# Optimization experiments

Measured on AMD Instinct MI355X. Metric: run time of the kernel, lower is better.

The kernel has to match this reference:

```python
import jax, jax.numpy as jnp
import numpy as np

B, T, H, LD, FFN, TED = 4, 4096, 8, 128, 512, 2048
D = H * LD
LN_EPS = 1e-5


def setup_inputs() -> dict:
    key = jax.random.key(0)
    ks = jax.random.split(key, 8)
    s = lambda k, shape, sc=0.02: jax.random.normal(k, shape, jnp.float32) * sc
    return dict(
        x=s(ks[0], (B, T, D), 1.0),
        emb=s(ks[1], (B, TED), 1.0),
        W1=s(ks[2], (H, LD, FFN)),   # per-head linear1 weights
        b1=jnp.zeros((H, FFN), jnp.float32),
        W2=s(ks[3], (H, FFN, LD)),   # per-head linear2 weights
        b2=jnp.zeros((H, LD), jnp.float32),
        ln_w=jnp.ones((D,), jnp.float32),
        ln_b=jnp.zeros((D,), jnp.float32),
        emb_W=s(ks[4], (TED, 2 * D)),
        emb_b=jnp.zeros((2 * D,), jnp.float32),
        out_W=s(ks[5], (D, D)),
        out_b=jnp.zeros((D,), jnp.float32),
    )


def reference(x, emb, W1, b1, W2, b2, ln_w, ln_b, emb_W, emb_b, out_W, out_b):
    Bx, Tx, Dx = x.shape
    Hx = W1.shape[0]
    xh = x.reshape(Bx, Tx, Hx, -1)                      # (B,T,H,ld)
    # batched per-head 2-layer MLP (replaces the Python loop over heads)
    h1 = jax.nn.gelu(jnp.einsum('bthd,hdf->bthf', xh, W1) + b1, approximate=False)
    y = jnp.einsum('bthf,hfd->bthd', h1, W2) + b2       # (B,T,H,ld)
    y = y.reshape(Bx, Tx, Dx)                            # concat over heads
    # StylizationBlock: SiLU -> Linear -> scale/shift; LN modulate; SiLU -> Linear
    emb_out = jax.nn.silu(emb) @ emb_W + emb_b           # (B, 2D)
    scale, shift = jnp.split(emb_out[:, None, :], 2, axis=-1)
    mu = jnp.mean(y, axis=-1, keepdims=True)
    var = jnp.var(y, axis=-1, keepdims=True)
    yn = (y - mu) * jax.lax.rsqrt(var + LN_EPS) * ln_w + ln_b
    h = yn * (1.0 + scale) + shift
    out = jax.nn.silu(h) @ out_W + out_b
    return x + out
```

## Files before the change

### kernel.cpp

```cpp
#include <hip/hip_runtime.h>
#include <hip/hip_bf16.h>
#include <math.h>

#define B_     4
#define T_     4096
#define H_     8
#define LD_    128
#define FFN_   512
#define D_     1024
#define TED_   2048
#define TWO_D_ 2048
#define NTOK_  (B_ * T_)
#define LN_EPS_ 1e-5f

#define WS_EMB_OFF   0
#define WS_IMG1_OFF  (64 * 1024)
#define WS_IMG2_OFF  ((64 << 10) + (1 << 20))
#define WS_IMGO_OFF  ((64 << 10) + (2 << 20))
#define WS_Y_OFF     (8 << 20)

typedef short bf16x8 __attribute__((ext_vector_type(8)));
typedef float f32x4  __attribute__((ext_vector_type(4)));
typedef float f32x16 __attribute__((ext_vector_type(16)));
typedef unsigned int u32x4 __attribute__((ext_vector_type(4)));

__device__ __forceinline__ float siluf(float v) {
  return v * __builtin_amdgcn_rcpf(1.0f + __expf(-v));
}
__device__ __forceinline__ float geluf(float v) {
  const float s  = v * 0.70710678118654752440f;
  const float ax = fabsf(s);
  const float t  = __builtin_amdgcn_rcpf(fmaf(0.3275911f, ax, 1.0f));
  const float e  = __expf(-ax * ax);
  float p = fmaf(1.061405429f, t, -1.453152027f);
  p = fmaf(p, t, 1.421413741f);
  p = fmaf(p, t, -0.284496736f);
  p = fmaf(p, t, 0.254829592f);
  p = p * t;
  const float erf_ax = fmaf(-p, e, 1.0f);
  const float erf_s  = copysignf(erf_ax, s);
  return 0.5f * v * (1.0f + erf_s);
}
__device__ __forceinline__ unsigned short f2bf(float v) {
  unsigned int u = __float_as_uint(v);
  u += 0x7fffu + ((u >> 16) & 1u);
  return (unsigned short)(u >> 16);
}
__device__ __forceinline__ unsigned int pack2(float a, float b) {
  return (unsigned int)f2bf(a) | ((unsigned int)f2bf(b) << 16);
}
__device__ __forceinline__ void unpack8(uint4 u, float* v) {
  v[0] = __uint_as_float(u.x << 16); v[1] = __uint_as_float(u.x & 0xffff0000u);
  v[2] = __uint_as_float(u.y << 16); v[3] = __uint_as_float(u.y & 0xffff0000u);
  v[4] = __uint_as_float(u.z << 16); v[5] = __uint_as_float(u.z & 0xffff0000u);
  v[6] = __uint_as_float(u.w << 16); v[7] = __uint_as_float(u.w & 0xffff0000u);
}

__device__ __forceinline__ void gload_lds16(const void* g, void* l) {
#pragma clang diagnostic push
#pragma clang diagnostic ignored "-Waddress-space-conversion"
  __builtin_amdgcn_global_load_lds(
      (const __attribute__((address_space(1))) unsigned int*)g,
      (__attribute__((address_space(3))) unsigned int*)l, 16, 0, 0);
#pragma clang diagnostic pop
}

__global__ __launch_bounds__(256) void k0_emb(
    const float* __restrict__ emb, const float* __restrict__ emb_W,
    const float* __restrict__ emb_b, float* __restrict__ emb_out) {
  __shared__ float se[B_][128];
  const int tid = threadIdx.x;
  const int j   = blockIdx.x * 256 + tid;
  const int k0  = blockIdx.y * 128;
  for (int i = tid; i < B_ * 128; i += 256) {
    const int b = i >> 7, k = i & 127;
    se[b][k] = siluf(emb[b * TED_ + k0 + k]);
  }
  __syncthreads();
  float a0 = 0.f, a1 = 0.f, a2 = 0.f, a3 = 0.f;
  const float* Wp = emb_W + (size_t)k0 * TWO_D_ + j;
  for (int k = 0; k < 128; ++k) {
    const float w = Wp[(size_t)k * TWO_D_];
    a0 += se[0][k] * w; a1 += se[1][k] * w;
    a2 += se[2][k] * w; a3 += se[3][k] * w;
  }
  if (blockIdx.y == 0) {
    const float bb = emb_b[j];
    a0 += bb; a1 += bb; a2 += bb; a3 += bb;
  }
  atomicAdd(&emb_out[0 * TWO_D_ + j], a0);
  atomicAdd(&emb_out[1 * TWO_D_ + j], a1);
  atomicAdd(&emb_out[2 * TWO_D_ + j], a2);
  atomicAdd(&emb_out[3 * TWO_D_ + j], a3);
}

__global__ __launch_bounds__(256) void kprep(
    const float* __restrict__ W1, const float* __restrict__ W2,
    const float* __restrict__ out_W,
    unsigned short* __restrict__ img1, unsigned short* __restrict__ img2,
    unsigned short* __restrict__ imgO) {
  const int t = blockIdx.x;
  const int tid = threadIdx.x;
  if (t < 64) {
    const bool is1 = (t < 32);
    const int h = (t & 31) >> 2, q = t & 3;
    const int l = tid & 63, fg = tid >> 6;
    const int l31 = l & 31, hi8 = (l >> 5) * 8;
    #pragma unroll
    for (int i = 0; i < 8; ++i) {
      const int fid = fg * 8 + i;
      float val[8];
      size_t dsto;
      if (is1) {
        const int c = q * 4 + (fid >> 3), kb = fid & 7;
        const float* sp = W1 + (size_t)h * 65536 +
                          (size_t)(kb * 16 + hi8) * 512 + c * 32 + l31;
        #pragma unroll
        for (int j = 0; j < 8; ++j) val[j] = sp[(size_t)j * 512];
        dsto = (size_t)h * 65536 + (size_t)(c * 8 + kb) * 512 + l * 8;
      } else {
        const int c = q * 4 + (fid >> 3), kb2 = (fid >> 2) & 1, nt = fid & 3;
        const float* sp = W2 + (size_t)h * 65536 +
                          (size_t)(c * 32 + kb2 * 16 + hi8) * 128 + nt * 32 + l31;
        #pragma unroll
        for (int j = 0; j < 8; ++j) val[j] = sp[(size_t)j * 128];
        dsto = (size_t)h * 65536 + (size_t)(c * 8 + kb2 * 4 + nt) * 512 + l * 8;
      }
      unsigned int p[4];
      #pragma unroll
      for (int qq = 0; qq < 4; ++qq) p[qq] = pack2(val[2 * qq], val[2 * qq + 1]);
      *reinterpret_cast<uint4*>((is1 ? img1 : img2) + dsto) =
          make_uint4(p[0], p[1], p[2], p[3]);
    }
    return;
  }
  __shared__ float ls[128][129];
  const int tt = t - 64, tr = tt >> 3, tc = tt & 7;
  const float* src = out_W + (size_t)tr * 128 * 1024 + tc * 128;
  unsigned short* dst = imgO + (size_t)tc * 128 * 1024 + tr * 128;
  for (int i = tid; i < 128 * 32; i += 256) {
    const int r = i >> 5, c4 = (i & 31) << 2;
    const float4 v = *reinterpret_cast<const float4*>(src + (size_t)r * 1024 + c4);
    ls[r][c4] = v.x; ls[r][c4 + 1] = v.y; ls[r][c4 + 2] = v.z; ls[r][c4 + 3] = v.w;
  }
  __syncthreads();
  for (int u = tid; u < 2048; u += 256) {
    const int nn = u >> 4, kb = (u & 15) << 3;
    unsigned int p[4];
    #pragma unroll
    for (int qq = 0; qq < 4; ++qq)
      p[qq] = pack2(ls[kb + 2 * qq][nn], ls[kb + 2 * qq + 1][nn]);
    *reinterpret_cast<uint4*>(dst + (size_t)nn * 1024 + kb) =
        make_uint4(p[0], p[1], p[2], p[3]);
  }
}

__global__ __launch_bounds__(256, 3) void k1_mfma(
    const float* __restrict__ x,
    const unsigned short* __restrict__ img1,
    const unsigned short* __restrict__ img2,
    const float* __restrict__ b1, const float* __restrict__ b2,
    unsigned short* __restrict__ y) {
  __shared__ unsigned short wbuf[2][16 * 512];
  const int h = blockIdx.y;
  const int tid = threadIdx.x, w = tid >> 6, l = tid & 63;
  const int t0 = blockIdx.x * 128 + w * 32;
  const int l31 = l & 31, hi = l >> 5;

  const unsigned short* s1 = img1 + ((size_t)h << 16);
  const unsigned short* s2 = img2 + ((size_t)h << 16);

  auto stage = [&](unsigned short* buf, int c) {
    #pragma unroll
    for (int i = 0; i < 4; ++i) {
      const int slot = w * 4 + i;
      const unsigned short* src = (slot < 8)
          ? (s1 + (size_t)(c * 8 + slot) * 512 + l * 8)
          : (s2 + (size_t)(c * 8 + (slot - 8)) * 512 + l * 8);
      gload_lds16(src, buf + slot * 512);
    }
  };

  bf16x8 xf[8];
  {
    const float* xr = x + (size_t)(t0 + l31) * D_ + h * LD_ + hi * 8;
    #pragma unroll
    for (int kb = 0; kb < 8; ++kb) {
      const float4 a = *reinterpret_cast<const float4*>(xr + kb * 16);
      const float4 b = *reinterpret_cast<const float4*>(xr + kb * 16 + 4);
      bf16x8 f;
      f[0] = (short)f2bf(a.x); f[1] = (short)f2bf(a.y);
      f[2] = (short)f2bf(a.z); f[3] = (short)f2bf(a.w);
      f[4] = (short)f2bf(b.x); f[5] = (short)f2bf(b.y);
      f[6] = (short)f2bf(b.z); f[7] = (short)f2bf(b.w);
      xf[kb] = f;
    }
  }

  f32x16 acc2[4];
  #pragma unroll
  for (int nt = 0; nt < 4; ++nt)
    #pragma unroll
    for (int r = 0; r < 16; ++r) acc2[nt][r] = 0.f;

  auto compute = [&](const unsigned short* buf, int c) {
    f32x16 acc1;
    #pragma unroll
    for (int r = 0; r < 16; ++r) acc1[r] = 0.f;
    #pragma unroll
    for (int kb = 0; kb < 8; ++kb) {
      const bf16x8 a = *reinterpret_cast<const bf16x8*>(buf + kb * 512 + l * 8);
      acc1 = __builtin_amdgcn_mfma_f32_32x32x16_bf16(a, xf[kb], acc1, 0, 0, 0);
    }
    float g[16];
    #pragma unroll
    for (int q = 0; q < 4; ++q) {
      const float4 bq = *reinterpret_cast<const float4*>(
          b1 + h * FFN_ + c * 32 + q * 8 + hi * 4);
      g[q*4+0] = geluf(acc1[q*4+0] + bq.x);
      g[q*4+1] = geluf(acc1[q*4+1] + bq.y);
      g[q*4+2] = geluf(acc1[q*4+2] + bq.z);
      g[q*4+3] = geluf(acc1[q*4+3] + bq.w);
    }
    unsigned int P[4][2];
    #pragma unroll
    for (int q = 0; q < 4; ++q) {
      P[q][0] = pack2(g[q*4+0], g[q*4+1]);
      P[q][1] = pack2(g[q*4+2], g[q*4+3]);
    }
    unsigned int A2[2][4];
    #pragma unroll
    for (int half = 0; half < 2; ++half) {
      const int qe = half * 2, qo = half * 2 + 1;
      #pragma unroll
      for (int s = 0; s < 2; ++s) {
        const unsigned int offer = hi ? P[qe][s] : P[qo][s];
        const unsigned int recv =
            (unsigned int)__shfl_xor((int)offer, 32);
        A2[half][s]     = hi ? recv : P[qe][s];
        A2[half][s + 2] = hi ? P[qo][s] : recv;
      }
    }
    #pragma unroll
    for (int kb2 = 0; kb2 < 2; ++kb2) {
      u32x4 t;
      t[0] = A2[kb2][0]; t[1] = A2[kb2][1];
      t[2] = A2[kb2][2]; t[3] = A2[kb2][3];
      const bf16x8 a2 = __builtin_bit_cast(bf16x8, t);
      #pragma unroll
      for (int nt = 0; nt < 4; ++nt) {
        const bf16x8 b2f = *reinterpret_cast<const bf16x8*>(
            buf + (8 + kb2 * 4 + nt) * 512 + l * 8);
        acc2[nt] = __builtin_amdgcn_mfma_f32_32x32x16_bf16(a2, b2f, acc2[nt], 0, 0, 0);
      }
    }
  };

  stage(wbuf[0], 0);
  __syncthreads();
  #pragma unroll 1
  for (int c = 0; c < 16; c += 2) {
    if (c + 1 < 16) stage(wbuf[1], c + 1);
    compute(wbuf[0], c);
    __syncthreads();
    if (c + 2 < 16) stage(wbuf[0], c + 2);
    compute(wbuf[1], c + 1);
    __syncthreads();
  }

  #pragma unroll
  for (int nt = 0; nt < 4; ++nt) {
    const int d = nt * 32 + l31;
    const float bb = b2[h * LD_ + d];
    #pragma unroll
    for (int r = 0; r < 16; ++r) {
      const int tq = t0 + (r & 3) + 8 * (r >> 2) + 4 * hi;
      y[(size_t)tq * D_ + h * LD_ + d] = f2bf(acc2[nt][r] + bb);
    }
  }
}

__global__ __launch_bounds__(256) void k2_ln(
    unsigned short* __restrict__ y, const float* __restrict__ ln_w,
    const float* __restrict__ ln_b, const float* __restrict__ emb_out) {
  const int tid = threadIdx.x;
  const int bt  = blockIdx.x * 4 + (tid >> 6);
  const int l   = tid & 63;
  const int b   = bt >> 12;
  unsigned short* rowp = y + (size_t)bt * D_ + l * 16;
  const uint4 u0 = *reinterpret_cast<const uint4*>(rowp);
  const uint4 u1 = *reinterpret_cast<const uint4*>(rowp + 8);
  float v[16];
  unpack8(u0, v); unpack8(u1, v + 8);
  float s = 0.f, s2 = 0.f;
  #pragma unroll
  for (int j = 0; j < 16; ++j) { s += v[j]; s2 += v[j] * v[j]; }
  #pragma unroll
  for (int off = 1; off < 64; off <<= 1) {
    s  += __shfl_xor(s, off);
    s2 += __shfl_xor(s2, off);
  }
  const float mu   = s * (1.0f / D_);
  const float rstd = rsqrtf(s2 * (1.0f / D_) - mu * mu + LN_EPS_);
  const int d0 = l * 16;
  float r[16];
  #pragma unroll
  for (int q = 0; q < 4; ++q) {
    const float4 lw = *reinterpret_cast<const float4*>(ln_w + d0 + q * 4);
    const float4 lb = *reinterpret_cast<const float4*>(ln_b + d0 + q * 4);
    const float4 sc = *reinterpret_cast<const float4*>(emb_out + (size_t)b * TWO_D_ + d0 + q * 4);
    const float4 sh = *reinterpret_cast<const float4*>(emb_out + (size_t)b * TWO_D_ + D_ + d0 + q * 4);
    r[q*4+0] = siluf(((v[q*4+0] - mu) * rstd * lw.x + lb.x) * (1.f + sc.x) + sh.x);
    r[q*4+1] = siluf(((v[q*4+1] - mu) * rstd * lw.y + lb.y) * (1.f + sc.y) + sh.y);
    r[q*4+2] = siluf(((v[q*4+2] - mu) * rstd * lw.z + lb.z) * (1.f + sc.z) + sh.z);
    r[q*4+3] = siluf(((v[q*4+3] - mu) * rstd * lw.w + lb.w) * (1.f + sc.w) + sh.w);
  }
  uint4 o0, o1;
  o0.x = pack2(r[0], r[1]);  o0.y = pack2(r[2], r[3]);
  o0.z = pack2(r[4], r[5]);  o0.w = pack2(r[6], r[7]);
  o1.x = pack2(r[8], r[9]);  o1.y = pack2(r[10], r[11]);
  o1.z = pack2(r[12], r[13]); o1.w = pack2(r[14], r[15]);
  *reinterpret_cast<uint4*>(rowp)     = o0;
  *reinterpret_cast<uint4*>(rowp + 8) = o1;
}

__global__ __launch_bounds__(256) void k3_mfma(
    const unsigned short* __restrict__ hb,
    const unsigned short* __restrict__ imgO,
    const float* __restrict__ out_b, const float* __restrict__ x,
    float* __restrict__ out) {
  __shared__ unsigned short As[128 * 32];
  __shared__ unsigned short Bs[128 * 32];
  const int bid = blockIdx.x;
  const int swz = (bid & 7) * 128 + (bid >> 3);
  const int m0 = (swz >> 3) * 128;
  const int n0 = (swz & 7) * 128;
  const int tid = threadIdx.x, w = tid >> 6, l = tid & 63;
  const int lr = l & 15, lg = l >> 4;
  const int wm0 = (w & 1) * 64, wn0 = (w >> 1) * 64;

  f32x4 acc[4][4];
  #pragma unroll
  for (int mf = 0; mf < 4; ++mf)
    #pragma unroll
    for (int nf = 0; nf < 4; ++nf)
      acc[mf][nf] = (f32x4){0.f, 0.f, 0.f, 0.f};

  const int srow = (l >> 2);
  const int scol = (l & 3) * 8;
  for (int kc = 0; kc < 32; ++kc) {
    #pragma unroll
    for (int i = 0; i < 2; ++i) {
      const int c = w * 2 + i;
      const int row = c * 16 + srow;
      gload_lds16(hb   + (size_t)(m0 + row) * D_ + kc * 32 + scol, &As[c * 512]);
      gload_lds16(imgO + (size_t)(n0 + row) * D_ + kc * 32 + scol, &Bs[c * 512]);
    }
    __syncthreads();
    bf16x8 af[4], bf[4];
    #pragma unroll
    for (int mf = 0; mf < 4; ++mf)
      af[mf] = *reinterpret_cast<const bf16x8*>(&As[(wm0 + mf * 16 + lr) * 32 + lg * 8]);
    #pragma unroll
    for (int nf = 0; nf < 4; ++nf)
      bf[nf] = *reinterpret_cast<const bf16x8*>(&Bs[(wn0 + nf * 16 + lr) * 32 + lg * 8]);
    #pragma unroll
    for (int mf = 0; mf < 4; ++mf)
      #pragma unroll
      for (int nf = 0; nf < 4; ++nf)
        acc[mf][nf] = __builtin_amdgcn_mfma_f32_16x16x32_bf16(af[mf], bf[nf], acc[mf][nf], 0, 0, 0);
    __syncthreads();
  }

  #pragma unroll
  for (int mf = 0; mf < 4; ++mf) {
    #pragma unroll
    for (int nf = 0; nf < 4; ++nf) {
      const int n = n0 + wn0 + nf * 16 + lr;
      const float bb = out_b[n];
      #pragma unroll
      for (int r = 0; r < 4; ++r) {
        const int m = m0 + wm0 + mf * 16 + lg * 4 + r;
        out[(size_t)m * D_ + n] = acc[mf][nf][r] + bb + x[(size_t)m * D_ + n];
      }
    }
  }
}

extern "C" void kernel_launch(void* const* d_in, const int* in_sizes, int n_in,
                              void* d_out, int out_size, void* d_ws, size_t ws_size,
                              hipStream_t stream) {
  const float* x     = (const float*)d_in[0];
  const float* emb   = (const float*)d_in[1];
  const float* W1    = (const float*)d_in[2];
  const float* b1    = (const float*)d_in[3];
  const float* W2    = (const float*)d_in[4];
  const float* b2    = (const float*)d_in[5];
  const float* ln_w  = (const float*)d_in[6];
  const float* ln_b  = (const float*)d_in[7];
  const float* emb_W = (const float*)d_in[8];
  const float* emb_b = (const float*)d_in[9];
  const float* out_W = (const float*)d_in[10];
  const float* out_b = (const float*)d_in[11];
  float* out = (float*)d_out;

  float*          emb_out = (float*)((char*)d_ws + WS_EMB_OFF);
  unsigned short* img1    = (unsigned short*)((char*)d_ws + WS_IMG1_OFF);
  unsigned short* img2    = (unsigned short*)((char*)d_ws + WS_IMG2_OFF);
  unsigned short* imgO    = (unsigned short*)((char*)d_ws + WS_IMGO_OFF);
  unsigned short* ybuf    = (unsigned short*)((char*)d_ws + WS_Y_OFF);

  hipMemsetAsync(emb_out, 0, B_ * TWO_D_ * sizeof(float), stream);
  k0_emb<<<dim3(TWO_D_ / 256, 16), 256, 0, stream>>>(emb, emb_W, emb_b, emb_out);
  kprep<<<128, 256, 0, stream>>>(W1, W2, out_W, img1, img2, imgO);
  k1_mfma<<<dim3(NTOK_ / 128, H_), 256, 0, stream>>>(x, img1, img2, b1, b2, ybuf);
  k2_ln<<<NTOK_ / 4, 256, 0, stream>>>(ybuf, ln_w, ln_b, emb_out);
  k3_mfma<<<1024, 256, 0, stream>>>(ybuf, imgO, out_b, x, out);
}
```

Measured before the change: 178.4 us.

## Merge emb and weight-prep kernels, widen k1 blocks, use hardware bf16 pack

Fuses the embedding projection kernel into the weight-prep kernel as extra blocks, removing one launch. Doubles the k1 block to 512 threads (8 waves, 256 tokens), so each staged weight chunk in LDS is shared by twice as many waves and each wave issues half the loads. Replaces the software round-to-nearest bf16 conversion with the v_cvt_pk_bf16_f32 instruction in the pack paths. The larger block with launch_bounds(512,4) may raise register pressure or reduce the number of blocks resident per CU.

```diff
diff --git a/kernel.cpp b/kernel.cpp
--- a/kernel.cpp
+++ b/kernel.cpp
@@ -47,7 +47,9 @@
   return (unsigned short)(u >> 16);
 }
 __device__ __forceinline__ unsigned int pack2(float a, float b) {
-  return (unsigned int)f2bf(a) | ((unsigned int)f2bf(b) << 16);
+  unsigned int r;
+  asm("v_cvt_pk_bf16_f32 %0, %1, %2" : "=v"(r) : "v"(a), "v"(b));
+  return r;
 }
 __device__ __forceinline__ void unpack8(uint4 u, float* v) {
   v[0] = __uint_as_float(u.x << 16); v[1] = __uint_as_float(u.x & 0xffff0000u);
@@ -65,40 +67,13 @@
 #pragma clang diagnostic pop
 }
 
-__global__ __launch_bounds__(256) void k0_emb(
-    const float* __restrict__ emb, const float* __restrict__ emb_W,
-    const float* __restrict__ emb_b, float* __restrict__ emb_out) {
-  __shared__ float se[B_][128];
-  const int tid = threadIdx.x;
-  const int j   = blockIdx.x * 256 + tid;
-  const int k0  = blockIdx.y * 128;
-  for (int i = tid; i < B_ * 128; i += 256) {
-    const int b = i >> 7, k = i & 127;
-    se[b][k] = siluf(emb[b * TED_ + k0 + k]);
-  }
-  __syncthreads();
-  float a0 = 0.f, a1 = 0.f, a2 = 0.f, a3 = 0.f;
-  const float* Wp = emb_W + (size_t)k0 * TWO_D_ + j;
-  for (int k = 0; k < 128; ++k) {
-    const float w = Wp[(size_t)k * TWO_D_];
-    a0 += se[0][k] * w; a1 += se[1][k] * w;
-    a2 += se[2][k] * w; a3 += se[3][k] * w;
-  }
-  if (blockIdx.y == 0) {
-    const float bb = emb_b[j];
-    a0 += bb; a1 += bb; a2 += bb; a3 += bb;
-  }
-  atomicAdd(&emb_out[0 * TWO_D_ + j], a0);
-  atomicAdd(&emb_out[1 * TWO_D_ + j], a1);
-  atomicAdd(&emb_out[2 * TWO_D_ + j], a2);
-  atomicAdd(&emb_out[3 * TWO_D_ + j], a3);
-}
-
-__global__ __launch_bounds__(256) void kprep(
+__global__ __launch_bounds__(256) void kinit(
     const float* __restrict__ W1, const float* __restrict__ W2,
     const float* __restrict__ out_W,
+    const float* __restrict__ emb, const float* __restrict__ emb_W,
+    const float* __restrict__ emb_b,
     unsigned short* __restrict__ img1, unsigned short* __restrict__ img2,
-    unsigned short* __restrict__ imgO) {
+    unsigned short* __restrict__ imgO, float* __restrict__ emb_out) {
   const int t = blockIdx.x;
   const int tid = threadIdx.x;
   if (t < 64) {
@@ -134,28 +109,57 @@
     }
     return;
   }
-  __shared__ float ls[128][129];
-  const int tt = t - 64, tr = tt >> 3, tc = tt & 7;
-  const float* src = out_W + (size_t)tr * 128 * 1024 + tc * 128;
-  unsigned short* dst = imgO + (size_t)tc * 128 * 1024 + tr * 128;
-  for (int i = tid; i < 128 * 32; i += 256) {
-    const int r = i >> 5, c4 = (i & 31) << 2;
-    const float4 v = *reinterpret_cast<const float4*>(src + (size_t)r * 1024 + c4);
-    ls[r][c4] = v.x; ls[r][c4 + 1] = v.y; ls[r][c4 + 2] = v.z; ls[r][c4 + 3] = v.w;
-  }
-  __syncthreads();
-  for (int u = tid; u < 2048; u += 256) {
-    const int nn = u >> 4, kb = (u & 15) << 3;
-    unsigned int p[4];
-    #pragma unroll
-    for (int qq = 0; qq < 4; ++qq)
-      p[qq] = pack2(ls[kb + 2 * qq][nn], ls[kb + 2 * qq + 1][nn]);
-    *reinterpret_cast<uint4*>(dst + (size_t)nn * 1024 + kb) =
-        make_uint4(p[0], p[1], p[2], p[3]);
-  }
-}
-
-__global__ __launch_bounds__(256, 3) void k1_mfma(
+  if (t < 128) {
+    __shared__ float ls[128][129];
+    const int tt = t - 64, tr = tt >> 3, tc = tt & 7;
+    const float* src = out_W + (size_t)tr * 128 * 1024 + tc * 128;
+    unsigned short* dst = imgO + (size_t)tc * 128 * 1024 + tr * 128;
+    for (int i = tid; i < 128 * 32; i += 256) {
+      const int r = i >> 5, c4 = (i & 31) << 2;
+      const float4 v = *reinterpret_cast<const float4*>(src + (size_t)r * 1024 + c4);
+      ls[r][c4] = v.x; ls[r][c4 + 1] = v.y; ls[r][c4 + 2] = v.z; ls[r][c4 + 3] = v.w;
+    }
+    __syncthreads();
+    for (int u = tid; u < 2048; u += 256) {
+      const int nn = u >> 4, kb = (u & 15) << 3;
+      unsigned int p[4];
+      #pragma unroll
+      for (int qq = 0; qq < 4; ++qq)
+        p[qq] = pack2(ls[kb + 2 * qq][nn], ls[kb + 2 * qq + 1][nn]);
+      *reinterpret_cast<uint4*>(dst + (size_t)nn * 1024 + kb) =
+          make_uint4(p[0], p[1], p[2], p[3]);
+    }
+    return;
+  }
+  {
+    __shared__ float se[B_][128];
+    const int bid = t - 128;
+    const int j   = (bid & 7) * 256 + tid;
+    const int k0  = (bid >> 3) * 128;
+    for (int i = tid; i < B_ * 128; i += 256) {
+      const int b = i >> 7, k = i & 127;
+      se[b][k] = siluf(emb[b * TED_ + k0 + k]);
+    }
+    __syncthreads();
+    float a0 = 0.f, a1 = 0.f, a2 = 0.f, a3 = 0.f;
+    const float* Wp = emb_W + (size_t)k0 * TWO_D_ + j;
+    for (int k = 0; k < 128; ++k) {
+      const float w = Wp[(size_t)k * TWO_D_];
+      a0 += se[0][k] * w; a1 += se[1][k] * w;
+      a2 += se[2][k] * w; a3 += se[3][k] * w;
+    }
+    if ((bid >> 3) == 0) {
+      const float bb = emb_b[j];
+      a0 += bb; a1 += bb; a2 += bb; a3 += bb;
+    }
+    atomicAdd(&emb_out[0 * TWO_D_ + j], a0);
+    atomicAdd(&emb_out[1 * TWO_D_ + j], a1);
+    atomicAdd(&emb_out[2 * TWO_D_ + j], a2);
+    atomicAdd(&emb_out[3 * TWO_D_ + j], a3);
+  }
+}
+
+__global__ __launch_bounds__(512, 4) void k1_mfma(
     const float* __restrict__ x,
     const unsigned short* __restrict__ img1,
     const unsigned short* __restrict__ img2,
@@ -164,7 +168,7 @@
   __shared__ unsigned short wbuf[2][16 * 512];
   const int h = blockIdx.y;
   const int tid = threadIdx.x, w = tid >> 6, l = tid & 63;
-  const int t0 = blockIdx.x * 128 + w * 32;
+  const int t0 = blockIdx.x * 256 + w * 32;
   const int l31 = l & 31, hi = l >> 5;
 
   const unsigned short* s1 = img1 + ((size_t)h << 16);
@@ -172,8 +176,8 @@
 
   auto stage = [&](unsigned short* buf, int c) {
     #pragma unroll
-    for (int i = 0; i < 4; ++i) {
-      const int slot = w * 4 + i;
+    for (int i = 0; i < 2; ++i) {
+      const int slot = w * 2 + i;
       const unsigned short* src = (slot < 8)
           ? (s1 + (size_t)(c * 8 + slot) * 512 + l * 8)
           : (s2 + (size_t)(c * 8 + (slot - 8)) * 512 + l * 8);
@@ -188,12 +192,10 @@
     for (int kb = 0; kb < 8; ++kb) {
       const float4 a = *reinterpret_cast<const float4*>(xr + kb * 16);
       const float4 b = *reinterpret_cast<const float4*>(xr + kb * 16 + 4);
-      bf16x8 f;
-      f[0] = (short)f2bf(a.x); f[1] = (short)f2bf(a.y);
-      f[2] = (short)f2bf(a.z); f[3] = (short)f2bf(a.w);
-      f[4] = (short)f2bf(b.x); f[5] = (short)f2bf(b.y);
-      f[6] = (short)f2bf(b.z); f[7] = (short)f2bf(b.w);
-      xf[kb] = f;
+      u32x4 u;
+      u[0] = pack2(a.x, a.y); u[1] = pack2(a.z, a.w);
+      u[2] = pack2(b.x, b.y); u[3] = pack2(b.z, b.w);
+      xf[kb] = __builtin_bit_cast(bf16x8, u);
     }
   }
 
@@ -273,9 +275,13 @@
     const int d = nt * 32 + l31;
     const float bb = b2[h * LD_ + d];
     #pragma unroll
-    for (int r = 0; r < 16; ++r) {
-      const int tq = t0 + (r & 3) + 8 * (r >> 2) + 4 * hi;
-      y[(size_t)tq * D_ + h * LD_ + d] = f2bf(acc2[nt][r] + bb);
+    for (int rp = 0; rp < 8; ++rp) {
+      const int r0 = 2 * rp, r1 = 2 * rp + 1;
+      const unsigned int pk = pack2(acc2[nt][r0] + bb, acc2[nt][r1] + bb);
+      const int tA = t0 + (r0 & 3) + 8 * (r0 >> 2) + 4 * hi;
+      const int tB = tA + 1;
+      y[(size_t)tA * D_ + h * LD_ + d] = (unsigned short)(pk & 0xffffu);
+      y[(size_t)tB * D_ + h * LD_ + d] = (unsigned short)(pk >> 16);
     }
   }
 }
@@ -411,9 +417,9 @@
   unsigned short* ybuf    = (unsigned short*)((char*)d_ws + WS_Y_OFF);
 
   hipMemsetAsync(emb_out, 0, B_ * TWO_D_ * sizeof(float), stream);
-  k0_emb<<<dim3(TWO_D_ / 256, 16), 256, 0, stream>>>(emb, emb_W, emb_b, emb_out);
-  kprep<<<128, 256, 0, stream>>>(W1, W2, out_W, img1, img2, imgO);
-  k1_mfma<<<dim3(NTOK_ / 128, H_), 256, 0, stream>>>(x, img1, img2, b1, b2, ybuf);
+  kinit<<<256, 256, 0, stream>>>(W1, W2, out_W, emb, emb_W, emb_b,
+                                 img1, img2, imgO, emb_out);
+  k1_mfma<<<dim3(NTOK_ / 256, H_), 512, 0, stream>>>(x, img1, img2, b1, b2, ybuf);
   k2_ln<<<NTOK_ / 4, 256, 0, stream>>>(ybuf, ln_w, ln_b, emb_out);
   k3_mfma<<<1024, 256, 0, stream>>>(ybuf, imgO, out_b, x, out);
 }
```

New measurement: 192.3 us. +7.8%, slower.
